# Kernel tuning notes

Hardware: AMD Instinct MI355X
Metric: run time of the kernel (lower is better)

The kernel has to match this reference:

```python
import jax, jax.numpy as jnp
import numpy as np

N_HEADS = 16
WINDOW = 128
EPS = 1e-6
NEG_INF = -1e30  # effectively -inf after softmax in fp32


def setup_inputs() -> dict:
    key = jax.random.key(0)
    ks = jax.random.split(key, 5)
    B, T, D = 2, 2048, 1024
    scale = 1.0 / np.sqrt(D)
    return {
        "x": jax.random.normal(ks[0], (B, T, D), dtype=jnp.float32),
        "Wq": jax.random.normal(ks[1], (D, D), dtype=jnp.float32) * scale,
        "Wk": jax.random.normal(ks[2], (D, D), dtype=jnp.float32) * scale,
        "Wv": jax.random.normal(ks[3], (D, D), dtype=jnp.float32) * scale,
        "Wo": jax.random.normal(ks[4], (D, D), dtype=jnp.float32) * scale,
    }


def _l2norm(t):
    # torch F.normalize: t / max(||t||, eps)
    n = jnp.sqrt(jnp.sum(t * t, axis=-1, keepdims=True))
    return t / jnp.maximum(n, EPS)


def reference(x, Wq, Wk, Wv, Wo):
    B, T, D = x.shape
    H, hd = N_HEADS, D // N_HEADS
    # projections (torch Linear: x @ W.T), split heads -> [B, H, T, hd]
    def proj(W):
        return jnp.einsum('btd,ed->bte', x, W).reshape(B, T, H, hd).transpose(0, 2, 1, 3)
    q = _l2norm(proj(Wq))
    k = _l2norm(proj(Wk))
    v = proj(Wv)
    # scores [B, H, T, T] (no 1/sqrt(d) scale in the source)
    attn = jnp.einsum('bhqd,bhkd->bhqk', q, k)
    pos = jnp.arange(T)
    rel = pos[None, :] - pos[:, None]            # rel[i, j] = j - i
    mask = (rel < 0) | (rel >= WINDOW)           # allowed: 0 <= j-i < window
    base = jnp.linspace(0.0, 1.0, H, dtype=x.dtype)
    slopes = jnp.power(jnp.asarray(2.0, x.dtype), -(8.0 * base))  # [H]
    alibi = -jnp.abs(rel).astype(x.dtype)[None, :, :] * slopes[:, None, None]  # [H,T,T]
    bias = jnp.where(mask[None, :, :], jnp.asarray(NEG_INF, x.dtype), alibi)
    attn = jax.nn.softmax(attn + bias[None], axis=-1)
    out = jnp.einsum('bhqk,bhkd->bhqd', attn, v)
    out = out.transpose(0, 2, 1, 3).reshape(B, T, D)
    return jnp.einsum('btd,ed->bte', out, Wo)
```

## Files before the change

### kernel.cpp

```cpp
#include <hip/hip_runtime.h>
#include <hip/hip_bf16.h>

#define T_SEQ   2048
#define BATCH   2
#define DMODEL  1024
#define NHEADS  16
#define HDIM    64
#define WINDOW  128

typedef __attribute__((ext_vector_type(8))) short bf16x8;
typedef __attribute__((ext_vector_type(4))) float f32x4;

__device__ inline void unpack8(uint4 u, float* f) {
    unsigned int w[4] = {u.x, u.y, u.z, u.w};
#pragma unroll
    for (int i = 0; i < 4; i++) {
        f[2*i]   = __uint_as_float(w[i] << 16);
        f[2*i+1] = __uint_as_float(w[i] & 0xffff0000u);
    }
}

__device__ inline void gld_lds16(const __hip_bfloat16* g, __hip_bfloat16* l) {
    __builtin_amdgcn_global_load_lds(
        (const __attribute__((address_space(1))) unsigned int*)g,
        (__attribute__((address_space(3))) unsigned int*)l, 16, 0, 0);
}

__global__ __launch_bounds__(256) void cvt_kernel(
    const float* __restrict__ x,  const float* __restrict__ Wq,
    const float* __restrict__ Wk, const float* __restrict__ Wv,
    const float* __restrict__ Wo,
    __hip_bfloat16* __restrict__ xb, __hip_bfloat16* __restrict__ Wb)
{
    const int slot = blockIdx.y;
    const float* src;
    __hip_bfloat16* dst;
    int n;
    if (slot == 0) { src = x; dst = xb; n = 4 * 1024 * 1024; }
    else {
        src = (slot == 1) ? Wq : (slot == 2) ? Wk : (slot == 3) ? Wv : Wo;
        dst = Wb + (size_t)(slot - 1) * 1024 * 1024;
        n = 1024 * 1024;
    }
    int i = (blockIdx.x * 256 + threadIdx.x) * 8;
    if (i >= n) return;
    float4 a = *(const float4*)(src + i);
    float4 b = *(const float4*)(src + i + 4);
    __hip_bfloat16 pk[8] = {
        __float2bfloat16(a.x), __float2bfloat16(a.y),
        __float2bfloat16(a.z), __float2bfloat16(a.w),
        __float2bfloat16(b.x), __float2bfloat16(b.y),
        __float2bfloat16(b.z), __float2bfloat16(b.w)};
    *(uint4*)(dst + i) = *(uint4*)pk;
}

template<bool C_F32>
__global__ __launch_bounds__(256) void gemm_bt_bf16(
    const __hip_bfloat16* __restrict__ A,
    const __hip_bfloat16* __restrict__ W0,
    const __hip_bfloat16* __restrict__ W1,
    const __hip_bfloat16* __restrict__ W2,
    void* __restrict__ C0v, void* __restrict__ C1v, void* __restrict__ C2v,
    int M, int N, int K)
{
    const int z = blockIdx.z;
    const __hip_bfloat16* W = (z == 0) ? W0 : (z == 1 ? W1 : W2);
    void* Cv = (z == 0) ? C0v : (z == 1 ? C1v : C2v);

    const int n0 = blockIdx.x * 128;
    const int m0 = blockIdx.y * 128;

    __shared__ __hip_bfloat16 As[128 * 32];
    __shared__ __hip_bfloat16 Bs[128 * 32];

    const int t    = threadIdx.x;
    const int lane = t & 63;
    const int wv   = t >> 6;

    const int srow = wv * 32 + (lane >> 2);
    const int gc   = ((lane & 3) - (lane >> 3)) & 3;
    const __hip_bfloat16* Ag = A + (size_t)(m0 + srow) * K + gc * 8;
    const __hip_bfloat16* Wg = W + (size_t)(n0 + srow) * K + gc * 8;
    const size_t row16 = (size_t)16 * K;
    __hip_bfloat16* AsD0 = &As[(wv * 32) * 32];
    __hip_bfloat16* AsD1 = &As[(wv * 32 + 16) * 32];
    __hip_bfloat16* BsD0 = &Bs[(wv * 32) * 32];
    __hip_bfloat16* BsD1 = &Bs[(wv * 32 + 16) * 32];

    const int wm   = (wv >> 1) * 64;
    const int wn   = (wv & 1) * 64;
    const int lrow = lane & 15;
    const int quad = lane >> 4;
    const int slot = ((quad + (lrow >> 1)) & 3) * 8;

    f32x4 acc[4][4];
#pragma unroll
    for (int i = 0; i < 4; i++)
#pragma unroll
        for (int j = 0; j < 4; j++)
            acc[i][j] = (f32x4){0.f, 0.f, 0.f, 0.f};

    for (int k0 = 0; k0 < K; k0 += 32) {
        gld_lds16(Ag + k0,         AsD0);
        gld_lds16(Ag + k0 + row16, AsD1);
        gld_lds16(Wg + k0,         BsD0);
        gld_lds16(Wg + k0 + row16, BsD1);
        __syncthreads();

        bf16x8 af[4], bfv[4];
#pragma unroll
        for (int mi = 0; mi < 4; mi++)
            af[mi] = *(const bf16x8*)&As[(wm + mi * 16 + lrow) * 32 + slot];
#pragma unroll
        for (int ni = 0; ni < 4; ni++)
            bfv[ni] = *(const bf16x8*)&Bs[(wn + ni * 16 + lrow) * 32 + slot];
#pragma unroll
        for (int mi = 0; mi < 4; mi++)
#pragma unroll
            for (int ni = 0; ni < 4; ni++)
                acc[mi][ni] = __builtin_amdgcn_mfma_f32_16x16x32_bf16(
                    af[mi], bfv[ni], acc[mi][ni], 0, 0, 0);
        __syncthreads();
    }

#pragma unroll
    for (int mi = 0; mi < 4; mi++) {
#pragma unroll
        for (int rr = 0; rr < 4; rr++) {
            int row = m0 + wm + mi * 16 + quad * 4 + rr;
            if (C_F32) {
                float* Crow = (float*)Cv + (size_t)row * N + n0 + wn + lrow;
#pragma unroll
                for (int ni = 0; ni < 4; ni++)
                    Crow[ni * 16] = acc[mi][ni][rr];
            } else {
                __hip_bfloat16* Crow = (__hip_bfloat16*)Cv + (size_t)row * N + n0 + wn + lrow;
#pragma unroll
                for (int ni = 0; ni < 4; ni++)
                    Crow[ni * 16] = __float2bfloat16(acc[mi][ni][rr]);
            }
        }
    }
}

__global__ __launch_bounds__(256) void l2norm_kernel(__hip_bfloat16* Q, __hip_bfloat16* Kb)
{
    int gw   = (blockIdx.x * 256 + threadIdx.x) >> 6;
    int lane = threadIdx.x & 63;
    __hip_bfloat16* buf = (gw < 4096) ? Q : Kb;
    int row = gw & 4095;
    __hip_bfloat16* p = buf + (size_t)row * DMODEL + lane * 16;

    uint4 u0 = *(uint4*)p;
    uint4 u1 = *(uint4*)(p + 8);
    float v[16];
    unpack8(u0, v);
    unpack8(u1, v + 8);
    float ss = 0.f;
#pragma unroll
    for (int i = 0; i < 16; i++) ss += v[i] * v[i];
    ss += __shfl_xor(ss, 1);
    ss += __shfl_xor(ss, 2);
    float inv = 1.0f / fmaxf(sqrtf(ss), 1e-6f);
    __hip_bfloat16 pk[16];
#pragma unroll
    for (int i = 0; i < 16; i++) pk[i] = __float2bfloat16(v[i] * inv);
    *(uint4*)p       = *(uint4*)pk;
    *(uint4*)(p + 8) = *(uint4*)(pk + 8);
}

__global__ __launch_bounds__(256) void attn_kernel(
    const __hip_bfloat16* __restrict__ Q,
    const __hip_bfloat16* __restrict__ K,
    const __hip_bfloat16* __restrict__ V,
    __hip_bfloat16* __restrict__ O)
{
    const int i0 = blockIdx.x * 64;
    const int h  = blockIdx.y;
    const int b  = blockIdx.z;

    __shared__ __hip_bfloat16 Ks[192 * 72];
    __shared__ __hip_bfloat16 Vt[64 * 208];

    const size_t base = ((size_t)b * T_SEQ) * DMODEL + h * HDIM;
    const int t = threadIdx.x;

    for (int task = t; task < 192 * 8; task += 256) {
        int row = task >> 3;
        int c   = task & 7;
        int j   = min(i0 + row, T_SEQ - 1);
        *(uint4*)&Ks[row * 72 + c * 8] = *(const uint4*)(K + base + (size_t)j * DMODEL + c * 8);
        uint4 vv = *(const uint4*)(V + base + (size_t)j * DMODEL + c * 8);
        __hip_bfloat16 tmp[8];
        *(uint4*)tmp = vv;
#pragma unroll
        for (int e = 0; e < 8; e++)
            Vt[(c * 8 + e) * 208 + row] = tmp[e];
    }
    for (int task = t; task < 64 * 16; task += 256) {
        int rw = task >> 4, cc = task & 15;
        Vt[rw * 208 + 192 + cc] = __float2bfloat16(0.f);
    }
    __syncthreads();

    const int lane = t & 63;
    const int w    = t >> 6;
    const int col  = lane & 15;
    const int quad = lane >> 4;
    const float slope = exp2f(-8.0f * (float)h / 15.0f);

    const __hip_bfloat16* qp = Q + base + (size_t)(i0 + w * 16 + col) * DMODEL + quad * 8;
    bf16x8 qf0 = *(const bf16x8*)(qp);
    bf16x8 qf1 = *(const bf16x8*)(qp + 32);

    f32x4 sc[9];
#pragma unroll
    for (int kt = 0; kt < 9; kt++) {
        sc[kt] = (f32x4){0.f, 0.f, 0.f, 0.f};
        const __hip_bfloat16* kr = &Ks[(w * 16 + kt * 16 + col) * 72 + quad * 8];
        bf16x8 kb0 = *(const bf16x8*)(kr);
        bf16x8 kb1 = *(const bf16x8*)(kr + 32);
        sc[kt] = __builtin_amdgcn_mfma_f32_16x16x32_bf16(qf0, kb0, sc[kt], 0, 0, 0);
        sc[kt] = __builtin_amdgcn_mfma_f32_16x16x32_bf16(qf1, kb1, sc[kt], 0, 0, 0);
    }

    float mx[4] = {-3e38f, -3e38f, -3e38f, -3e38f};
#pragma unroll
    for (int kt = 0; kt < 9; kt++) {
#pragma unroll
        for (int r = 0; r < 4; r++) {
            int ql  = quad * 4 + r;
            int rel = kt * 16 + col - ql;
            int ka  = i0 + w * 16 + kt * 16 + col;
            bool valid = (rel >= 0) && (rel < WINDOW) && (ka < T_SEQ);
            float v = valid ? (sc[kt][r] - (float)rel * slope) : -1e30f;
            sc[kt][r] = v;
            mx[r] = fmaxf(mx[r], v);
        }
    }
#pragma unroll
    for (int r = 0; r < 4; r++) {
        mx[r] = fmaxf(mx[r], __shfl_xor(mx[r], 1));
        mx[r] = fmaxf(mx[r], __shfl_xor(mx[r], 2));
        mx[r] = fmaxf(mx[r], __shfl_xor(mx[r], 4));
        mx[r] = fmaxf(mx[r], __shfl_xor(mx[r], 8));
    }
    float sm[4] = {0.f, 0.f, 0.f, 0.f};
#pragma unroll
    for (int kt = 0; kt < 9; kt++) {
#pragma unroll
        for (int r = 0; r < 4; r++) {
            float e = __expf(sc[kt][r] - mx[r]);
            sc[kt][r] = e;
            sm[r] += e;
        }
    }
#pragma unroll
    for (int r = 0; r < 4; r++) {
        sm[r] += __shfl_xor(sm[r], 1);
        sm[r] += __shfl_xor(sm[r], 2);
        sm[r] += __shfl_xor(sm[r], 4);
        sm[r] += __shfl_xor(sm[r], 8);
        sm[r] = 1.0f / sm[r];
    }

    __syncthreads();
    __hip_bfloat16* Ps = Ks + w * (16 * 168);
#pragma unroll
    for (int kt = 0; kt < 9; kt++)
#pragma unroll
        for (int r = 0; r < 4; r++)
            Ps[(quad * 4 + r) * 168 + kt * 16 + col] = __float2bfloat16(sc[kt][r] * sm[r]);
#pragma unroll
    for (int i = 0; i < 4; i++)
        Ps[(lane & 15) * 168 + 144 + quad * 4 + i] = __float2bfloat16(0.f);
    __syncthreads();

    f32x4 o[4];
#pragma unroll
    for (int nd = 0; nd < 4; nd++) o[nd] = (f32x4){0.f, 0.f, 0.f, 0.f};
#pragma unroll
    for (int kc = 0; kc < 5; kc++) {
        bf16x8 pf = *(const bf16x8*)&Ps[col * 168 + kc * 32 + quad * 8];
#pragma unroll
        for (int nd = 0; nd < 4; nd++) {
            bf16x8 vf = *(const bf16x8*)&Vt[(nd * 16 + col) * 208 + w * 16 + kc * 32 + quad * 8];
            o[nd] = __builtin_amdgcn_mfma_f32_16x16x32_bf16(pf, vf, o[nd], 0, 0, 0);
        }
    }

#pragma unroll
    for (int r = 0; r < 4; r++) {
        __hip_bfloat16* op = O + base + (size_t)(i0 + w * 16 + quad * 4 + r) * DMODEL + col;
#pragma unroll
        for (int nd = 0; nd < 4; nd++)
            op[nd * 16] = __float2bfloat16(o[nd][r]);
    }
}

extern "C" void kernel_launch(void* const* d_in, const int* in_sizes, int n_in,
                              void* d_out, int out_size, void* d_ws, size_t ws_size,
                              hipStream_t stream)
{
    const float* x  = (const float*)d_in[0];
    const float* Wq = (const float*)d_in[1];
    const float* Wk = (const float*)d_in[2];
    const float* Wv = (const float*)d_in[3];
    const float* Wo = (const float*)d_in[4];
    float* out = (float*)d_out;

    const size_t MT = (size_t)BATCH * T_SEQ;
    __hip_bfloat16* Qw = (__hip_bfloat16*)d_ws;
    __hip_bfloat16* Kw = Qw + MT * DMODEL;
    __hip_bfloat16* Vw = Kw + MT * DMODEL;
    __hip_bfloat16* XA = Vw + MT * DMODEL;
    __hip_bfloat16* Wb = XA + MT * DMODEL;

    cvt_kernel<<<dim3(2048, 5), 256, 0, stream>>>(x, Wq, Wk, Wv, Wo, XA, Wb);

    dim3 g1(DMODEL / 128, MT / 128, 3);
    gemm_bt_bf16<false><<<g1, 256, 0, stream>>>(
        XA, Wb, Wb + 1024 * 1024, Wb + 2 * 1024 * 1024,
        Qw, Kw, Vw, (int)MT, DMODEL, DMODEL);

    l2norm_kernel<<<2048, 256, 0, stream>>>(Qw, Kw);

    dim3 g2(T_SEQ / 64, NHEADS, BATCH);
    attn_kernel<<<g2, 256, 0, stream>>>(Qw, Kw, Vw, XA);

    dim3 g3(DMODEL / 128, MT / 128, 1);
    gemm_bt_bf16<true><<<g3, 256, 0, stream>>>(
        XA, Wb + 3 * 1024 * 1024, Wb + 3 * 1024 * 1024, Wb + 3 * 1024 * 1024,
        out, out, out, (int)MT, DMODEL, DMODEL);
}
```

Baseline: 173.3 us.

## Fuse l2norm into QKV GEMM epilogue, swizzle V transpose, shrink output GEMM tile

Computes the per-head L2 normalisation of Q and K inside the projection GEMM epilogue using cross-lane shuffles, removing the separate l2norm kernel and its extra read/write of Q and K. The attention kernel's V transpose now gathers 8x8 blocks in registers and writes vectorised, XOR-swizzled rows into LDS, replacing scalar transposed stores. The output projection GEMM is templated to a 64-row M tile to launch more blocks. The trade-off is more epilogue shuffles and index arithmetic, plus lower per-block reuse in the output GEMM.

```diff
diff --git a/kernel.cpp b/kernel.cpp
--- a/kernel.cpp
+++ b/kernel.cpp
@@ -54,7 +54,7 @@
     *(uint4*)(dst + i) = *(uint4*)pk;
 }
 
-template<bool C_F32>
+template<bool C_F32, int MI>
 __global__ __launch_bounds__(256) void gemm_bt_bf16(
     const __hip_bfloat16* __restrict__ A,
     const __hip_bfloat16* __restrict__ W0,
@@ -68,54 +68,55 @@
     void* Cv = (z == 0) ? C0v : (z == 1 ? C1v : C2v);
 
     const int n0 = blockIdx.x * 128;
-    const int m0 = blockIdx.y * 128;
-
-    __shared__ __hip_bfloat16 As[128 * 32];
+    const int m0 = blockIdx.y * (MI * 32);
+
+    __shared__ __hip_bfloat16 As[MI * 32 * 32];
     __shared__ __hip_bfloat16 Bs[128 * 32];
 
     const int t    = threadIdx.x;
     const int lane = t & 63;
     const int wv   = t >> 6;
 
-    const int srow = wv * 32 + (lane >> 2);
-    const int gc   = ((lane & 3) - (lane >> 3)) & 3;
-    const __hip_bfloat16* Ag = A + (size_t)(m0 + srow) * K + gc * 8;
-    const __hip_bfloat16* Wg = W + (size_t)(n0 + srow) * K + gc * 8;
+    const int gc    = ((lane & 3) - (lane >> 3)) & 3;
+    const int srowA = wv * (MI * 8) + (lane >> 2);
+    const int srowB = wv * 32 + (lane >> 2);
+    const __hip_bfloat16* Ag = A + (size_t)(m0 + srowA) * K + gc * 8;
+    const __hip_bfloat16* Wg = W + (size_t)(n0 + srowB) * K + gc * 8;
     const size_t row16 = (size_t)16 * K;
-    __hip_bfloat16* AsD0 = &As[(wv * 32) * 32];
-    __hip_bfloat16* AsD1 = &As[(wv * 32 + 16) * 32];
+    __hip_bfloat16* AsD0 = &As[(wv * (MI * 8)) * 32];
+    __hip_bfloat16* AsD1 = &As[(wv * (MI * 8) + 16) * 32];
     __hip_bfloat16* BsD0 = &Bs[(wv * 32) * 32];
     __hip_bfloat16* BsD1 = &Bs[(wv * 32 + 16) * 32];
 
-    const int wm   = (wv >> 1) * 64;
+    const int wm   = (wv >> 1) * (MI * 16);
     const int wn   = (wv & 1) * 64;
     const int lrow = lane & 15;
     const int quad = lane >> 4;
     const int slot = ((quad + (lrow >> 1)) & 3) * 8;
 
-    f32x4 acc[4][4];
-#pragma unroll
-    for (int i = 0; i < 4; i++)
+    f32x4 acc[MI][4];
+#pragma unroll
+    for (int i = 0; i < MI; i++)
 #pragma unroll
         for (int j = 0; j < 4; j++)
             acc[i][j] = (f32x4){0.f, 0.f, 0.f, 0.f};
 
     for (int k0 = 0; k0 < K; k0 += 32) {
-        gld_lds16(Ag + k0,         AsD0);
-        gld_lds16(Ag + k0 + row16, AsD1);
+        gld_lds16(Ag + k0, AsD0);
+        if (MI == 4) gld_lds16(Ag + k0 + row16, AsD1);
         gld_lds16(Wg + k0,         BsD0);
         gld_lds16(Wg + k0 + row16, BsD1);
         __syncthreads();
 
-        bf16x8 af[4], bfv[4];
-#pragma unroll
-        for (int mi = 0; mi < 4; mi++)
+        bf16x8 af[MI], bfv[4];
+#pragma unroll
+        for (int mi = 0; mi < MI; mi++)
             af[mi] = *(const bf16x8*)&As[(wm + mi * 16 + lrow) * 32 + slot];
 #pragma unroll
         for (int ni = 0; ni < 4; ni++)
             bfv[ni] = *(const bf16x8*)&Bs[(wn + ni * 16 + lrow) * 32 + slot];
 #pragma unroll
-        for (int mi = 0; mi < 4; mi++)
+        for (int mi = 0; mi < MI; mi++)
 #pragma unroll
             for (int ni = 0; ni < 4; ni++)
                 acc[mi][ni] = __builtin_amdgcn_mfma_f32_16x16x32_bf16(
@@ -123,8 +124,29 @@
         __syncthreads();
     }
 
-#pragma unroll
-    for (int mi = 0; mi < 4; mi++) {
+    if (!C_F32 && z != 2) {
+#pragma unroll
+        for (int mi = 0; mi < MI; mi++) {
+#pragma unroll
+            for (int rr = 0; rr < 4; rr++) {
+                float ss = 0.f;
+#pragma unroll
+                for (int ni = 0; ni < 4; ni++)
+                    ss += acc[mi][ni][rr] * acc[mi][ni][rr];
+                ss += __shfl_xor(ss, 1);
+                ss += __shfl_xor(ss, 2);
+                ss += __shfl_xor(ss, 4);
+                ss += __shfl_xor(ss, 8);
+                float inv = 1.0f / fmaxf(sqrtf(ss), 1e-6f);
+#pragma unroll
+                for (int ni = 0; ni < 4; ni++)
+                    acc[mi][ni][rr] *= inv;
+            }
+        }
+    }
+
+#pragma unroll
+    for (int mi = 0; mi < MI; mi++) {
 #pragma unroll
         for (int rr = 0; rr < 4; rr++) {
             int row = m0 + wm + mi * 16 + quad * 4 + rr;
@@ -141,32 +163,6 @@
             }
         }
     }
-}
-
-__global__ __launch_bounds__(256) void l2norm_kernel(__hip_bfloat16* Q, __hip_bfloat16* Kb)
-{
-    int gw   = (blockIdx.x * 256 + threadIdx.x) >> 6;
-    int lane = threadIdx.x & 63;
-    __hip_bfloat16* buf = (gw < 4096) ? Q : Kb;
-    int row = gw & 4095;
-    __hip_bfloat16* p = buf + (size_t)row * DMODEL + lane * 16;
-
-    uint4 u0 = *(uint4*)p;
-    uint4 u1 = *(uint4*)(p + 8);
-    float v[16];
-    unpack8(u0, v);
-    unpack8(u1, v + 8);
-    float ss = 0.f;
-#pragma unroll
-    for (int i = 0; i < 16; i++) ss += v[i] * v[i];
-    ss += __shfl_xor(ss, 1);
-    ss += __shfl_xor(ss, 2);
-    float inv = 1.0f / fmaxf(sqrtf(ss), 1e-6f);
-    __hip_bfloat16 pk[16];
-#pragma unroll
-    for (int i = 0; i < 16; i++) pk[i] = __float2bfloat16(v[i] * inv);
-    *(uint4*)p       = *(uint4*)pk;
-    *(uint4*)(p + 8) = *(uint4*)(pk + 8);
 }
 
 __global__ __launch_bounds__(256) void attn_kernel(
@@ -180,7 +176,7 @@
     const int b  = blockIdx.z;
 
     __shared__ __hip_bfloat16 Ks[192 * 72];
-    __shared__ __hip_bfloat16 Vt[64 * 208];
+    __shared__ __hip_bfloat16 Vt[64 * 200 + 64];
 
     const size_t base = ((size_t)b * T_SEQ) * DMODEL + h * HDIM;
     const int t = threadIdx.x;
@@ -190,16 +186,31 @@
         int c   = task & 7;
         int j   = min(i0 + row, T_SEQ - 1);
         *(uint4*)&Ks[row * 72 + c * 8] = *(const uint4*)(K + base + (size_t)j * DMODEL + c * 8);
-        uint4 vv = *(const uint4*)(V + base + (size_t)j * DMODEL + c * 8);
-        __hip_bfloat16 tmp[8];
-        *(uint4*)tmp = vv;
-#pragma unroll
-        for (int e = 0; e < 8; e++)
-            Vt[(c * 8 + e) * 208 + row] = tmp[e];
-    }
-    for (int task = t; task < 64 * 16; task += 256) {
-        int rw = task >> 4, cc = task & 15;
-        Vt[rw * 208 + 192 + cc] = __float2bfloat16(0.f);
+    }
+    for (int task = t; task < 192; task += 256) {
+        int c  = task & 7;
+        int r0 = (task >> 3) * 8;
+        int b0 = task >> 3;
+        unsigned short m[8][8];
+#pragma unroll
+        for (int i = 0; i < 8; i++) {
+            int j = min(i0 + r0 + i, T_SEQ - 1);
+            uint4 u = *(const uint4*)(V + base + (size_t)j * DMODEL + c * 8);
+            unsigned short tmp[8];
+            *(uint4*)tmp = u;
+#pragma unroll
+            for (int e = 0; e < 8; e++) m[e][i] = tmp[e];
+        }
+#pragma unroll
+        for (int e = 0; e < 8; e++) {
+            int d  = c * 8 + e;
+            int sg = (b0 & ~7) | ((b0 + (d >> 3)) & 7);
+            *(uint4*)&Vt[d * 200 + sg * 8] = *(uint4*)m[e];
+        }
+    }
+    for (int task = t; task < 64; task += 256) {
+        uint4 zz = {0, 0, 0, 0};
+        *(uint4*)&Vt[task * 200 + 192] = zz;
     }
     __syncthreads();
 
@@ -282,9 +293,12 @@
 #pragma unroll
     for (int kc = 0; kc < 5; kc++) {
         bf16x8 pf = *(const bf16x8*)&Ps[col * 168 + kc * 32 + quad * 8];
+        int bblk = w * 2 + kc * 4 + quad;
 #pragma unroll
         for (int nd = 0; nd < 4; nd++) {
-            bf16x8 vf = *(const bf16x8*)&Vt[(nd * 16 + col) * 208 + w * 16 + kc * 32 + quad * 8];
+            int d  = nd * 16 + col;
+            int sg = (bblk < 24) ? ((bblk & ~7) | ((bblk + (d >> 3)) & 7)) : 24;
+            bf16x8 vf = *(const bf16x8*)&Vt[d * 200 + sg * 8];
             o[nd] = __builtin_amdgcn_mfma_f32_16x16x32_bf16(pf, vf, o[nd], 0, 0, 0);
         }
     }
@@ -319,17 +333,15 @@
     cvt_kernel<<<dim3(2048, 5), 256, 0, stream>>>(x, Wq, Wk, Wv, Wo, XA, Wb);
 
     dim3 g1(DMODEL / 128, MT / 128, 3);
-    gemm_bt_bf16<false><<<g1, 256, 0, stream>>>(
+    gemm_bt_bf16<false, 4><<<g1, 256, 0, stream>>>(
         XA, Wb, Wb + 1024 * 1024, Wb + 2 * 1024 * 1024,
         Qw, Kw, Vw, (int)MT, DMODEL, DMODEL);
 
-    l2norm_kernel<<<2048, 256, 0, stream>>>(Qw, Kw);
-
     dim3 g2(T_SEQ / 64, NHEADS, BATCH);
     attn_kernel<<<g2, 256, 0, stream>>>(Qw, Kw, Vw, XA);
 
-    dim3 g3(DMODEL / 128, MT / 128, 1);
-    gemm_bt_bf16<true><<<g3, 256, 0, stream>>>(
+    dim3 g3(DMODEL / 128, MT / 64, 1);
+    gemm_bt_bf16<true, 2><<<g3, 256, 0, stream>>>(
         XA, Wb + 3 * 1024 * 1024, Wb + 3 * 1024 * 1024, Wb + 3 * 1024 * 1024,
         out, out, out, (int)MT, DMODEL, DMODEL);
 }
```

Measured after the change: 158.0 us. -8.9%, faster.
